# Optimization experiments

Measured on AMD Instinct MI355X. Metric: run time of the kernel, lower is better.

## Reference

```python
import jax, jax.numpy as jnp
import numpy as np

RADIUS = 400.0
FIELD = 8000.0  # um extent of slide coordinate field


def setup_inputs() -> dict:
    key = jax.random.key(0)
    ks = jax.random.split(key, 8)
    B, N, D, H, K = 4, 4096, 1536, 512, 8
    images = jax.random.normal(ks[0], (B, N, D), dtype=jnp.float32)
    positions = jax.random.uniform(ks[1], (B, N, 2), dtype=jnp.float32) * FIELD
    W_feat = jax.random.normal(ks[2], (D, H), dtype=jnp.float32) * (1.0 / np.sqrt(D))
    b_feat = jnp.zeros((H,), dtype=jnp.float32)
    W_pos = jax.random.normal(ks[3], (2, H), dtype=jnp.float32) * 0.5
    W_gnn = jax.random.normal(ks[4], (H, H), dtype=jnp.float32) * (1.0 / np.sqrt(H))
    W_self = jax.random.normal(ks[5], (H, H), dtype=jnp.float32) * (1.0 / np.sqrt(H))
    anchors = jax.random.normal(ks[6], (K, D), dtype=jnp.float32)
    return {"images": images, "positions": positions, "W_feat": W_feat,
            "b_feat": b_feat, "W_pos": W_pos, "W_gnn": W_gnn,
            "W_self": W_self, "anchors": anchors}


def _radius_adjacency(pos):
    # pos: (N, 2). Dense O(N^2) radius graph (mirrors torch.cdist + mask).
    sq = jnp.sum(pos * pos, axis=-1)                       # (N,)
    d2 = sq[:, None] + sq[None, :] - 2.0 * (pos @ pos.T)   # (N, N)
    mask = d2 < (RADIUS * RADIUS)
    N = pos.shape[0]
    mask = mask & ~jnp.eye(N, dtype=bool)                  # no self-loops
    return mask.astype(pos.dtype)


def reference(images, positions, W_feat, b_feat, W_pos, W_gnn, W_self, anchors):
    # --- Stream A: explicit concept quantifier (cosine sim to anchors) ---
    x_norm = images / jnp.clip(jnp.linalg.norm(images, axis=-1, keepdims=True), 1e-12)
    a_norm = anchors / jnp.clip(jnp.linalg.norm(anchors, axis=-1, keepdims=True), 1e-12)
    scores = jnp.einsum('bnd,kd->bnk', x_norm, a_norm)     # (B, N, K)
    concept_profile = scores.mean(axis=1)                  # (B, K)

    # --- Stream B: feature extraction with positional encoding ---
    feat = images @ W_feat + b_feat + positions @ W_pos    # (B, N, H)

    # --- radius graph + one mean-aggregation GNN layer, per slide ---
    def per_graph(f, p):
        A = _radius_adjacency(p)                           # (N, N)
        deg = jnp.clip(A.sum(axis=-1, keepdims=True), 1.0) # (N, 1)
        h = jax.nn.relu(f)
        agg = (A @ h) / deg                                # mean over neighbors
        return jax.nn.relu(agg @ W_gnn + f @ W_self)       # (N, H)

    refined = jax.vmap(per_graph)(feat, positions)         # (B, N, H)
    latent_spatial = refined.mean(axis=1)                  # (B, H)  per-graph mean pool

    return jnp.concatenate([latent_spatial, concept_profile], axis=1)  # (B, H+K)
```

## Files before the change

### kernel.cpp

```cpp
#include <hip/hip_runtime.h>

#define B_ 4
#define N_ 4096
#define D_ 1536
#define H_ 512
#define K_ 8
#define M_ (B_*N_)
#define R2_ 160000.0f
#define CAP 192

typedef __attribute__((ext_vector_type(8))) short bf16x8;
typedef __attribute__((ext_vector_type(4))) float f32x4;
typedef __attribute__((ext_vector_type(2))) float f32x2;

__device__ __forceinline__ unsigned short f2bf(float f) {
  union { float f; unsigned u; } v; v.f = f;
  unsigned r = (v.u + 0x7FFFu + ((v.u >> 16) & 1u)) >> 16;
  return (unsigned short)r;
}

typedef const __attribute__((address_space(1))) unsigned int gas_u32;
typedef __attribute__((address_space(3))) unsigned int las_u32;
__device__ __forceinline__ void gl_lds16(const unsigned short* g, unsigned short* l) {
  __builtin_amdgcn_global_load_lds((gas_u32*)g, (las_u32*)l, 16, 0, 0);
}

#define CAST_BLKS 4096

__global__ __launch_bounds__(256) void k_prepcast(
    const float* __restrict__ images, const float* __restrict__ anchors,
    const float* __restrict__ Wf, const float* __restrict__ Wg, const float* __restrict__ Ws,
    unsigned short* __restrict__ imgs_bf, float* __restrict__ inv_norm,
    unsigned short* __restrict__ WfT, unsigned short* __restrict__ WgsT,
    unsigned short* __restrict__ ancT, float* __restrict__ invanorm) {
  int tid = threadIdx.x;
  if (blockIdx.x >= CAST_BLKS) {
    int bi = blockIdx.x - CAST_BLKS;
    if (bi < 320) {
      __shared__ float t[64][65];
      int bx = bi & 7, by = bi >> 3;
      const float* W; unsigned short* WT; int kt, outStride, outOff;
      if (by < 24)      { W = Wf; WT = WfT;  kt = by;      outStride = D_;   outOff = 0; }
      else if (by < 32) { W = Wg; WT = WgsT; kt = by - 24; outStride = 1024; outOff = 0; }
      else              { W = Ws; WT = WgsT; kt = by - 32; outStride = 1024; outOff = 512; }
      int tx = tid & 63, ty = tid >> 6;
      #pragma unroll
      for (int r = 0; r < 64; r += 4)
        t[ty + r][tx] = W[(size_t)(kt*64 + ty + r)*H_ + bx*64 + tx];
      __syncthreads();
      #pragma unroll
      for (int r = 0; r < 64; r += 4) {
        int n = bx*64 + ty + r;
        WT[(size_t)n*outStride + outOff + kt*64 + tx] = f2bf(t[tx][ty + r]);
      }
      return;
    }
    __shared__ float red[4];
    int k = bi - 320;
    float s = 0.f;
    for (int i = tid; i < D_; i += 256) {
      float v = anchors[k*D_ + i];
      s += v*v;
      ancT[(size_t)k*D_ + i] = f2bf(v);
      ancT[(size_t)(k+8)*D_ + i] = 0;
    }
    #pragma unroll
    for (int off = 32; off; off >>= 1) s += __shfl_down(s, off);
    if ((tid & 63) == 0) red[tid >> 6] = s;
    __syncthreads();
    if (tid == 0) invanorm[k] = 1.0f / fmaxf(sqrtf(red[0]+red[1]+red[2]+red[3]), 1e-12f);
    return;
  }
  int lane = tid & 63, w = tid >> 6;
  int row = blockIdx.x*4 + w;
  const float4* xr = (const float4*)(images + (size_t)row*D_);
  ushort4* ob = (ushort4*)(imgs_bf + (size_t)row*D_);
  float nrm = 0.f;
  #pragma unroll
  for (int it = 0; it < 6; it++) {
    float4 x = xr[lane + 64*it];
    nrm += x.x*x.x + x.y*x.y + x.z*x.z + x.w*x.w;
    ushort4 s;
    s.x = f2bf(x.x); s.y = f2bf(x.y); s.z = f2bf(x.z); s.w = f2bf(x.w);
    ob[lane + 64*it] = s;
  }
  #pragma unroll
  for (int off = 32; off; off >>= 1) nrm += __shfl_down(nrm, off);
  if (lane == 0) inv_norm[row] = 1.0f / fmaxf(sqrtf(nrm), 1e-12f);
}

#define BM 128
#define BN 128
#define BK 32

__global__ __launch_bounds__(256) void k_gemm(
    const unsigned short* __restrict__ A, const unsigned short* __restrict__ BT,
    int Kdim, int mode, const float* __restrict__ bias, const float* __restrict__ Wpos,
    const float* __restrict__ positions, unsigned short* __restrict__ AB,
    unsigned char* __restrict__ P, const unsigned short* __restrict__ ancT,
    const float* __restrict__ invnorm, const float* __restrict__ invanorm,
    float* __restrict__ out) {
  __shared__ __align__(16) unsigned short As[BM*BK];
  __shared__ unsigned short Bs[BN*BK];
  __shared__ float colsum[BN];
  int tid = threadIdx.x;
  int lane = tid & 63, wv = tid >> 6;
  int l15 = lane & 15, quad = lane >> 4;
  int bx = blockIdx.x;

  int wm = wv >> 1, wn = wv & 1;
  int j = bx >> 3;
  int bm = (bx & 7) + 8*(j >> 2), bn = j & 3;
  int m0 = bm*BM, n0 = bn*BN;

  const bool doC = (mode == 0) && (bn == 0);

  f32x4 acc[4][4] = {};
  f32x4 cacc[2] = {};
  const unsigned short* anc = ancT + l15*D_ + quad*8;

  int c = wv*2;
  int rowc = (lane >> 2), seg = lane & 3;
  const unsigned short* gA0 = A  + (size_t)(m0 + c*16 + rowc)*Kdim + seg*8;
  const unsigned short* gA1 = gA0 + (size_t)16*Kdim;
  const unsigned short* gB0 = BT + (size_t)(n0 + c*16 + rowc)*Kdim + seg*8;
  const unsigned short* gB1 = gB0 + (size_t)16*Kdim;
  unsigned short* lA0 = As + c*512;
  unsigned short* lA1 = lA0 + 512;
  unsigned short* lB0 = Bs + c*512;
  unsigned short* lB1 = lB0 + 512;

  int nk = Kdim / BK;
  for (int kt = 0; kt < nk; kt++) {
    __syncthreads();
    gl_lds16(gA0, lA0); gl_lds16(gA1, lA1);
    gl_lds16(gB0, lB0); gl_lds16(gB1, lB1);
    gA0 += BK; gA1 += BK; gB0 += BK; gB1 += BK;
    __syncthreads();

    bf16x8 aF[4], bF[4];
    #pragma unroll
    for (int f = 0; f < 4; f++)
      aF[f] = *(const bf16x8*)&As[(wm*64 + f*16 + l15)*BK + quad*8];
    #pragma unroll
    for (int f = 0; f < 4; f++)
      bF[f] = *(const bf16x8*)&Bs[(wn*64 + f*16 + l15)*BK + quad*8];
    #pragma unroll
    for (int mi = 0; mi < 4; mi++)
      #pragma unroll
      for (int ni = 0; ni < 4; ni++)
        acc[mi][ni] = __builtin_amdgcn_mfma_f32_16x16x32_bf16(aF[mi], bF[ni], acc[mi][ni], 0, 0, 0);

    if (doC) {
      bf16x8 ancF = *(const bf16x8*)anc;
      anc += BK;
      if (wn == 0) {
        cacc[0] = __builtin_amdgcn_mfma_f32_16x16x32_bf16(aF[0], ancF, cacc[0], 0, 0, 0);
        cacc[1] = __builtin_amdgcn_mfma_f32_16x16x32_bf16(aF[1], ancF, cacc[1], 0, 0, 0);
      } else {
        cacc[0] = __builtin_amdgcn_mfma_f32_16x16x32_bf16(aF[2], ancF, cacc[0], 0, 0, 0);
        cacc[1] = __builtin_amdgcn_mfma_f32_16x16x32_bf16(aF[3], ancF, cacc[1], 0, 0, 0);
      }
    }
  }

  if (doC) {
    float invA = (l15 < K_) ? invanorm[l15] : 0.f;
    float part = 0.f;
    #pragma unroll
    for (int f = 0; f < 2; f++) {
      const float4 q = *(const float4*)&invnorm[m0 + wm*64 + wn*32 + f*16 + quad*4];
      part += cacc[f][0]*q.x + cacc[f][1]*q.y + cacc[f][2]*q.z + cacc[f][3]*q.w;
    }
    part *= invA;
    part += __shfl_down(part, 32);
    part += __shfl_down(part, 16);
    if (lane < K_) atomicAdd(out + (m0 >> 12)*(H_+K_) + H_ + lane, part * (1.0f/N_));
  }

  if (mode == 0) {
    float bz[4], w0v[4], w1v[4];
    #pragma unroll
    for (int ni = 0; ni < 4; ni++) {
      int gh = n0 + wn*64 + ni*16 + l15;
      bz[ni] = bias[gh]; w0v[ni] = Wpos[gh]; w1v[ni] = Wpos[H_ + gh];
    }
    __syncthreads();
    float* sb = ((float*)As) + wv*256;
    int col4 = n0 + wn*64 + l15*4;
    #pragma unroll
    for (int mi = 0; mi < 4; mi++) {
      #pragma unroll
      for (int r = 0; r < 4; r++) {
        int gm = m0 + wm*64 + mi*16 + quad*4 + r;
        float2 p = ((const float2*)positions)[gm];
        #pragma unroll
        for (int ni = 0; ni < 4; ni++) {
          float v = acc[mi][ni][r] + bz[ni] + p.x*w0v[ni] + p.y*w1v[ni];
          sb[quad*64 + ni*16 + l15] = v;
        }
        f32x4 q = *(f32x4*)&sb[quad*64 + l15*4];
        uint2 o;
        o.x = ((unsigned)f2bf(q[1]) << 16) | f2bf(q[0]);
        o.y = ((unsigned)f2bf(q[3]) << 16) | f2bf(q[2]);
        *(uint2*)&AB[(size_t)gm*1024 + 512 + col4] = o;
        float e0 = fminf(fmaxf(q[0], 0.f)*0.015625f, 448.f);
        float e1 = fminf(fmaxf(q[1], 0.f)*0.015625f, 448.f);
        float e2 = fminf(fmaxf(q[2], 0.f)*0.015625f, 448.f);
        float e3 = fminf(fmaxf(q[3], 0.f)*0.015625f, 448.f);
        int u = __builtin_amdgcn_cvt_pk_fp8_f32(e0, e1, 0, false);
        u     = __builtin_amdgcn_cvt_pk_fp8_f32(e2, e3, u, true);
        *(unsigned*)(P + (size_t)gm*512 + col4) = (unsigned)u;
      }
    }
  } else {
    if (tid < BN) colsum[tid] = 0.f;
    __syncthreads();
    #pragma unroll
    for (int ni = 0; ni < 4; ni++) {
      float s = 0.f;
      #pragma unroll
      for (int mi = 0; mi < 4; mi++) {
        #pragma unroll
        for (int r = 0; r < 4; r++) s += fmaxf(acc[mi][ni][r], 0.f);
      }
      s += __shfl_down(s, 32);
      s += __shfl_down(s, 16);
      if (quad == 0) atomicAdd(&colsum[wn*64 + ni*16 + l15], s);
    }
    __syncthreads();
    if (tid < BN) {
      int b = m0 >> 12;
      atomicAdd(out + b*(H_+K_) + n0 + tid, colsum[tid] * (1.0f/N_));
    }
  }
}

__device__ __forceinline__ void accf8(uint2 v, float* a) {
  f32x2 p;
  p = __builtin_amdgcn_cvt_pk_f32_fp8(v.x, false); a[0] += p[0]; a[1] += p[1];
  p = __builtin_amdgcn_cvt_pk_f32_fp8(v.x, true);  a[2] += p[0]; a[3] += p[1];
  p = __builtin_amdgcn_cvt_pk_f32_fp8(v.y, false); a[4] += p[0]; a[5] += p[1];
  p = __builtin_amdgcn_cvt_pk_f32_fp8(v.y, true);  a[6] += p[0]; a[7] += p[1];
}

__global__ __launch_bounds__(256) void k_aggregate(const float* __restrict__ positions,
                                                   const unsigned char* __restrict__ P,
                                                   unsigned short* __restrict__ AB) {
  __shared__ unsigned short nl[8*CAP];
  __shared__ int cnt[8];
  __shared__ float sdx[8], sdy[8];
  int blk = blockIdx.x;
  int xcd = blk & 7;
  int b = xcd >> 1;
  int sub = ((blk >> 3) << 1) | (xcd & 1);
  int dest0 = sub * 8;
  int tid = threadIdx.x, lane = tid & 63, w = tid >> 6;
  const float2* p2 = (const float2*)(positions + (size_t)b*N_*2);
  if (tid < 8) {
    cnt[tid] = 0;
    float2 pd = p2[dest0 + tid];
    sdx[tid] = pd.x; sdy[tid] = pd.y;
  }
  __syncthreads();
  for (int it = 0; it < 16; it++) {
    int j = tid + 256*it;
    float2 pj = p2[j];
    #pragma unroll
    for (int d = 0; d < 8; d++) {
      float dx = pj.x - sdx[d], dy = pj.y - sdy[d];
      if (dx*dx + dy*dy < R2_ && j != dest0 + d) {
        int p = atomicAdd(&cnt[d], 1);
        if (p < CAP) nl[d*CAP + p] = (unsigned short)j;
      }
    }
  }
  __syncthreads();
  const unsigned char* featb = P + ((size_t)(b << 12))*512 + lane*8;
  #pragma unroll
  for (int dd = 0; dd < 2; dd++) {
    int d = w*2 + dd;
    int deg = cnt[d]; if (deg > CAP) deg = CAP;
    float inv = 64.0f / (float)(deg > 1 ? deg : 1);
    const unsigned short* nlp = &nl[d*CAP];
    float a[8] = {};
    int n = 0;
    for (; n + 4 <= deg; n += 4) {
      ushort4 idx = *(const ushort4*)&nlp[n];
      uint2 v0 = *(const uint2*)(featb + (size_t)idx.x*512);
      uint2 v1 = *(const uint2*)(featb + (size_t)idx.y*512);
      uint2 v2 = *(const uint2*)(featb + (size_t)idx.z*512);
      uint2 v3 = *(const uint2*)(featb + (size_t)idx.w*512);
      accf8(v0, a); accf8(v1, a); accf8(v2, a); accf8(v3, a);
    }
    for (; n < deg; n++) {
      int j = nlp[n];
      uint2 v = *(const uint2*)(featb + (size_t)j*512);
      accf8(v, a);
    }
    uint4 o;
    o.x = ((unsigned)f2bf(a[1]*inv) << 16) | f2bf(a[0]*inv);
    o.y = ((unsigned)f2bf(a[3]*inv) << 16) | f2bf(a[2]*inv);
    o.z = ((unsigned)f2bf(a[5]*inv) << 16) | f2bf(a[4]*inv);
    o.w = ((unsigned)f2bf(a[7]*inv) << 16) | f2bf(a[6]*inv);
    *(uint4*)(AB + (size_t)((b << 12) + dest0 + d)*1024 + lane*8) = o;
  }
}

extern "C" void kernel_launch(void* const* d_in, const int* in_sizes, int n_in,
                              void* d_out, int out_size, void* d_ws, size_t ws_size,
                              hipStream_t stream) {
  const float* images    = (const float*)d_in[0];
  const float* positions = (const float*)d_in[1];
  const float* W_feat    = (const float*)d_in[2];
  const float* b_feat    = (const float*)d_in[3];
  const float* W_pos     = (const float*)d_in[4];
  const float* W_gnn     = (const float*)d_in[5];
  const float* W_self    = (const float*)d_in[6];
  const float* anchors   = (const float*)d_in[7];
  float* out = (float*)d_out;

  char* ws = (char*)d_ws;
  unsigned short* imgs_bf = (unsigned short*)ws;
  unsigned short* AB      = (unsigned short*)(ws + 50331648);
  unsigned short* WfT     = (unsigned short*)(ws + 83886080);
  unsigned short* WgsT    = (unsigned short*)(ws + 85458944);
  unsigned char*  P       = (unsigned char*)(ws + 86507520);
  float*          invanorm= (float*)(ws + 94896128);
  unsigned short* ancT    = (unsigned short*)(ws + 94896160);
  float*          inv_norm= (float*)(ws + 94945312);

  hipMemsetAsync(d_out, 0, sizeof(float)*B_*(H_+K_), stream);
  k_prepcast<<<CAST_BLKS + 320 + 8, 256, 0, stream>>>(images, anchors, W_feat, W_gnn, W_self,
                                                      imgs_bf, inv_norm, WfT, WgsT, ancT, invanorm);
  k_gemm<<<512, 256, 0, stream>>>(imgs_bf, WfT, D_, 0, b_feat, W_pos, positions, AB, P,
                                  ancT, inv_norm, invanorm, out);
  k_aggregate<<<2048, 256, 0, stream>>>(positions, P, AB);
  k_gemm<<<512, 256, 0, stream>>>(AB, WgsT, 1024, 1, nullptr, nullptr, nullptr, AB, nullptr,
                                  ancT, inv_norm, invanorm, out);
}
```

Measured before the change: 285.9 us.

## Double-buffer LDS tiles in the bf16 MFMA GEMM to overlap loads with compute

The GEMM's shared-memory A/B tiles become two ping-pong buffers. The next K-slice is issued via global_load_lds into the idle buffer before the MFMAs on the current one run, which cuts the loop from two barriers per iteration to one. This aims to hide global-to-LDS latency behind the matrix math. It doubles the tile LDS footprint, which can lower occupancy. The end-of-loop barrier likely waits on the outstanding DMA, which limits how much overlap is actually gained.

```diff
diff --git a/kernel.cpp b/kernel.cpp
--- a/kernel.cpp
+++ b/kernel.cpp
@@ -100,8 +100,8 @@
     unsigned char* __restrict__ P, const unsigned short* __restrict__ ancT,
     const float* __restrict__ invnorm, const float* __restrict__ invanorm,
     float* __restrict__ out) {
-  __shared__ __align__(16) unsigned short As[BM*BK];
-  __shared__ unsigned short Bs[BN*BK];
+  __shared__ __align__(16) unsigned short As[2][BM*BK];
+  __shared__ __align__(16) unsigned short Bs[2][BN*BK];
   __shared__ float colsum[BN];
   int tid = threadIdx.x;
   int lane = tid & 63, wv = tid >> 6;
@@ -125,26 +125,32 @@
   const unsigned short* gA1 = gA0 + (size_t)16*Kdim;
   const unsigned short* gB0 = BT + (size_t)(n0 + c*16 + rowc)*Kdim + seg*8;
   const unsigned short* gB1 = gB0 + (size_t)16*Kdim;
-  unsigned short* lA0 = As + c*512;
-  unsigned short* lA1 = lA0 + 512;
-  unsigned short* lB0 = Bs + c*512;
-  unsigned short* lB1 = lB0 + 512;
 
   int nk = Kdim / BK;
+  gl_lds16(gA0, As[0] + c*512); gl_lds16(gA1, As[0] + c*512 + 512);
+  gl_lds16(gB0, Bs[0] + c*512); gl_lds16(gB1, Bs[0] + c*512 + 512);
+  gA0 += BK; gA1 += BK; gB0 += BK; gB1 += BK;
+  __syncthreads();
+
+  int cur = 0;
   for (int kt = 0; kt < nk; kt++) {
-    __syncthreads();
-    gl_lds16(gA0, lA0); gl_lds16(gA1, lA1);
-    gl_lds16(gB0, lB0); gl_lds16(gB1, lB1);
-    gA0 += BK; gA1 += BK; gB0 += BK; gB1 += BK;
-    __syncthreads();
-
+    if (kt + 1 < nk) {
+      unsigned short* nA = As[cur ^ 1] + c*512;
+      unsigned short* nB = Bs[cur ^ 1] + c*512;
+      gl_lds16(gA0, nA); gl_lds16(gA1, nA + 512);
+      gl_lds16(gB0, nB); gl_lds16(gB1, nB + 512);
+      gA0 += BK; gA1 += BK; gB0 += BK; gB1 += BK;
+    }
+
+    const unsigned short* Ab = As[cur];
+    const unsigned short* Bb = Bs[cur];
     bf16x8 aF[4], bF[4];
     #pragma unroll
     for (int f = 0; f < 4; f++)
-      aF[f] = *(const bf16x8*)&As[(wm*64 + f*16 + l15)*BK + quad*8];
+      aF[f] = *(const bf16x8*)&Ab[(wm*64 + f*16 + l15)*BK + quad*8];
     #pragma unroll
     for (int f = 0; f < 4; f++)
-      bF[f] = *(const bf16x8*)&Bs[(wn*64 + f*16 + l15)*BK + quad*8];
+      bF[f] = *(const bf16x8*)&Bb[(wn*64 + f*16 + l15)*BK + quad*8];
     #pragma unroll
     for (int mi = 0; mi < 4; mi++)
       #pragma unroll
@@ -162,6 +168,9 @@
         cacc[1] = __builtin_amdgcn_mfma_f32_16x16x32_bf16(aF[3], ancF, cacc[1], 0, 0, 0);
       }
     }
+
+    __syncthreads();
+    cur ^= 1;
   }
 
   if (doC) {
@@ -185,8 +194,7 @@
       int gh = n0 + wn*64 + ni*16 + l15;
       bz[ni] = bias[gh]; w0v[ni] = Wpos[gh]; w1v[ni] = Wpos[H_ + gh];
     }
-    __syncthreads();
-    float* sb = ((float*)As) + wv*256;
+    float* sb = ((float*)As[0]) + wv*256;
     int col4 = n0 + wn*64 + l15*4;
     #pragma unroll
     for (int mi = 0; mi < 4; mi++) {
```

Result: faster. 274.7 us (-3.9%).
